# Performance work log

Measured on AMD Instinct MI355X. Metric: run time of the kernel, lower is better.

Reference implementation:

```python
import jax, jax.numpy as jnp
import numpy as np

B, S, D, H = 4, 2048, 1024, 16
HD = D // H  # head_dim = 64


def setup_inputs() -> dict:
    key = jax.random.key(0)
    ks = jax.random.split(key, 5)
    scale = 1.0 / np.sqrt(D)
    return {
        "x": jax.random.normal(ks[0], (B, S, D), dtype=jnp.float32),
        "Wq": jax.random.normal(ks[1], (D, D), dtype=jnp.float32) * scale,
        "bq": jnp.zeros((D,), dtype=jnp.float32),
        "Wk": jax.random.normal(ks[2], (D, D), dtype=jnp.float32) * scale,
        "bk": jnp.zeros((D,), dtype=jnp.float32),
        "Wv": jax.random.normal(ks[3], (D, D), dtype=jnp.float32) * scale,
        "bv": jnp.zeros((D,), dtype=jnp.float32),
        "Wp": jax.random.normal(ks[4], (D, D), dtype=jnp.float32) * scale,
        "bp": jnp.zeros((D,), dtype=jnp.float32),
    }


def reference(x, Wq, bq, Wk, bk, Wv, bv, Wp, bp):
    b, s, d = x.shape
    # qkv projections (torch Linear: x @ W.T + b; here W stored as (in,out))
    q = (x @ Wq + bq).reshape(b, s, H, HD).transpose(0, 2, 1, 3)  # (b,h,s,hd)
    k = (x @ Wk + bk).reshape(b, s, H, HD).transpose(0, 2, 1, 3)
    v = (x @ Wv + bv).reshape(b, s, H, HD).transpose(0, 2, 1, 3)
    scores = jnp.einsum("bhqd,bhkd->bhqk", q, k) / np.sqrt(HD)
    causal = jnp.tril(jnp.ones((s, s), dtype=bool))
    scores = jnp.where(causal, scores, -jnp.inf)
    attn = jax.nn.softmax(scores, axis=-1)  # dropout is identity (p=0 / eval)
    out = jnp.einsum("bhqk,bhkd->bhqd", attn, v)
    out = out.transpose(0, 2, 1, 3).reshape(b, s, d)
    return out @ Wp + bp
```

## Files before the change

### kernel.cpp

```cpp
#include <hip/hip_runtime.h>

typedef __bf16 bf16;
typedef __attribute__((ext_vector_type(4))) __bf16 bf16x4;
typedef __attribute__((ext_vector_type(8))) __bf16 bf16x8;
typedef __attribute__((ext_vector_type(4))) float f32x4;
typedef __attribute__((ext_vector_type(4))) unsigned int u32x4;

#define B_ 4
#define S_ 2048
#define D_ 1024
#define H_ 16
#define HD_ 64

#define GLB(p) ((const __attribute__((address_space(1))) void*)(p))
#define LDS(p) ((__attribute__((address_space(3))) void*)(p))

__global__ __launch_bounds__(256) void transpose_cvt(
    const float* __restrict__ W0, const float* __restrict__ W1,
    const float* __restrict__ W2, const float* __restrict__ W3,
    bf16* __restrict__ T0, bf16* __restrict__ T1,
    bf16* __restrict__ T2, bf16* __restrict__ T3)
{
    __shared__ float tile[32][33];
    int z = blockIdx.z;
    const float* W = (z == 0) ? W0 : (z == 1) ? W1 : (z == 2) ? W2 : W3;
    bf16*        T = (z == 0) ? T0 : (z == 1) ? T1 : (z == 2) ? T2 : T3;
    int bx = blockIdx.x * 32, by = blockIdx.y * 32;
    int tx = threadIdx.x & 31, ty = threadIdx.x >> 5;
    #pragma unroll
    for (int j = 0; j < 32; j += 8)
        tile[ty + j][tx] = W[(size_t)(by + ty + j) * D_ + bx + tx];
    __syncthreads();
    #pragma unroll
    for (int j = 0; j < 32; j += 8)
        T[(size_t)(bx + ty + j) * D_ + by + tx] = (bf16)tile[tx][ty + j];
}

__global__ __launch_bounds__(256) void cvt_x(
    const float* __restrict__ X, bf16* __restrict__ Xb)
{
    size_t i = ((size_t)blockIdx.x * 256 + threadIdx.x) * 8;
    f32x4 a = *(const f32x4*)(X + i);
    f32x4 b = *(const f32x4*)(X + i + 4);
    bf16x8 v;
    #pragma unroll
    for (int j = 0; j < 4; ++j) { v[j] = (bf16)a[j]; v[4 + j] = (bf16)b[j]; }
    *(bf16x8*)(Xb + i) = v;
}

__global__ __launch_bounds__(256) void qkv_gemm(
    const bf16* __restrict__ Xb,
    const bf16* __restrict__ WqT, const bf16* __restrict__ WkT, const bf16* __restrict__ WvT,
    const float* __restrict__ bq, const float* __restrict__ bk, const float* __restrict__ bv,
    bf16* __restrict__ Qo, bf16* __restrict__ Ko, bf16* __restrict__ Vo)
{
    const int z = blockIdx.z;
    const bf16*  WT   = (z == 0) ? WqT : (z == 1) ? WkT : WvT;
    const float* bias = (z == 0) ? bq  : (z == 1) ? bk  : bv;
    bf16*        out  = (z == 0) ? Qo  : (z == 1) ? Ko  : Vo;
    const float scale = (z == 0) ? 0.18033688011112042f : 1.0f;

    __shared__ bf16 As[128 * 32];
    __shared__ bf16 Bs[128 * 32];

    const int t = threadIdx.x;
    const int lid = t & 63, w = t >> 6;
    const int wm = w & 1, wn = w >> 1;
    const int lrow = lid & 15, quad = lid >> 4;
    const int m0 = blockIdx.y * 128, n0 = blockIdx.x * 128;

    const bf16* Ag = Xb + (size_t)m0 * D_;
    const bf16* Bg = WT + (size_t)n0 * D_;

    const int row0 = t >> 2, k80 = (t & 3) << 3;
    const int row1 = (t + 256) >> 2;

    f32x4 acc[4][4] = {};

    for (int k0 = 0; k0 < D_; k0 += 32) {
        __syncthreads();
        __builtin_amdgcn_global_load_lds(GLB(Ag + (size_t)row0 * D_ + k0 + k80),
                                         LDS(As + t * 8), 16, 0, 0);
        __builtin_amdgcn_global_load_lds(GLB(Bg + (size_t)row0 * D_ + k0 + k80),
                                         LDS(Bs + t * 8), 16, 0, 0);
        __builtin_amdgcn_global_load_lds(GLB(Ag + (size_t)row1 * D_ + k0 + k80),
                                         LDS(As + t * 8 + 2048), 16, 0, 0);
        __builtin_amdgcn_global_load_lds(GLB(Bg + (size_t)row1 * D_ + k0 + k80),
                                         LDS(Bs + t * 8 + 2048), 16, 0, 0);
        __syncthreads();
        bf16x8 a[4], b[4];
        #pragma unroll
        for (int mb = 0; mb < 4; ++mb)
            a[mb] = *(const bf16x8*)(As + (wm * 64 + mb * 16 + lrow) * 32 + quad * 8);
        #pragma unroll
        for (int nb = 0; nb < 4; ++nb)
            b[nb] = *(const bf16x8*)(Bs + (wn * 64 + nb * 16 + lrow) * 32 + quad * 8);
        #pragma unroll
        for (int mb = 0; mb < 4; ++mb)
            #pragma unroll
            for (int nb = 0; nb < 4; ++nb)
                acc[mb][nb] = __builtin_amdgcn_mfma_f32_16x16x32_bf16(a[mb], b[nb], acc[mb][nb], 0, 0, 0);
    }

    #pragma unroll
    for (int mb = 0; mb < 4; ++mb) {
        #pragma unroll
        for (int nb = 0; nb < 4; ++nb) {
            int gn = n0 + wn * 64 + nb * 16 + lrow;
            float bsv = bias[gn];
            int h = gn >> 6, hd = gn & 63;
            int gm0 = m0 + wm * 64 + mb * 16 + quad * 4;
            int bb = gm0 >> 11, s0 = gm0 & 2047;
            if (z == 2) {
                bf16x4 pk;
                #pragma unroll
                for (int r = 0; r < 4; ++r)
                    pk[r] = (bf16)(acc[mb][nb][r] + bsv);
                *(bf16x4*)(out + (((size_t)(bb * H_ + h)) * HD_ + hd) * S_ + s0) = pk;
            } else {
                #pragma unroll
                for (int r = 0; r < 4; ++r) {
                    float v = (acc[mb][nb][r] + bsv) * scale;
                    out[(((size_t)(bb * H_ + h)) * S_ + (s0 + r)) * HD_ + hd] = (bf16)v;
                }
            }
        }
    }
}

__global__ __launch_bounds__(256) void attn_fwd(
    const bf16* __restrict__ Q, const bf16* __restrict__ K,
    const bf16* __restrict__ Vt, bf16* __restrict__ O)
{
    __shared__ bf16 Ks[64 * 64];
    __shared__ bf16 Vs[64 * 64];
    __shared__ bf16 Ps[4][16 * 64];

    const int lin = blockIdx.x + (blockIdx.y << 4);
    const int xcd = lin & 7;
    const int sl  = lin >> 3;
    const int bh  = xcd * 8 + (sl >> 4);
    const int bxp = sl & 15;

    const int t = threadIdx.x, lid = t & 63, w = t >> 6;
    const int lrow = lid & 15, quad = lid >> 4;
    const int b = bh >> 4, h = bh & 15;

    const int swz = (lrow & 7) << 4;

    const int srow0 = t >> 3, srow1 = srow0 + 32;
    const int k8 = (t & 7) << 3;
    const int sswz = ((t & 7) << 4) ^ ((srow0 & 7) << 4);
    char* kdst0 = (char*)Ks + srow0 * 128 + sswz;
    char* kdst1 = (char*)Ks + srow1 * 128 + sswz;
    char* vdst0 = (char*)Vs + srow0 * 128 + sswz;
    char* vdst1 = (char*)Vs + srow1 * 128 + sswz;

    bf16x8 onesv;
    #pragma unroll
    for (int j = 0; j < 8; ++j) onesv[j] = (bf16)1.0f;

    #pragma unroll 1
    for (int half = 0; half < 2; ++half) {
        const int qtile = half ? bxp : (31 - bxp);
        const int qbase = qtile * 64;

        const bf16* Qp = Q + ((size_t)bh * S_ + qbase + w * 16) * HD_;
        bf16x8 qf[2];
        #pragma unroll
        for (int ks = 0; ks < 2; ++ks)
            qf[ks] = *(const bf16x8*)(Qp + lrow * HD_ + ks * 32 + quad * 8);

        f32x4 o_acc[4] = {};
        f32x4 l_acc = {0.0f, 0.0f, 0.0f, 0.0f};
        float m_i = -3.0e4f;

        for (int kt = 0; kt <= qtile; ++kt) {
            const bf16* Kp = K  + ((size_t)bh * S_ + kt * 64) * HD_;
            const bf16* Vp = Vt + ((size_t)bh * HD_) * S_ + kt * 64;
            __syncthreads();
            u32x4 kv0 = *(const u32x4*)(Kp + (size_t)srow0 * HD_ + k8);
            u32x4 kv1 = *(const u32x4*)(Kp + (size_t)srow1 * HD_ + k8);
            u32x4 vv0 = *(const u32x4*)(Vp + (size_t)srow0 * S_ + k8);
            u32x4 vv1 = *(const u32x4*)(Vp + (size_t)srow1 * S_ + k8);
            *(u32x4*)kdst0 = kv0;
            *(u32x4*)kdst1 = kv1;
            *(u32x4*)vdst0 = vv0;
            *(u32x4*)vdst1 = vv1;
            __syncthreads();

            f32x4 sa[4] = {};
            #pragma unroll
            for (int ks = 0; ks < 2; ++ks) {
                const int ro = ((ks << 6) + (quad << 4)) ^ swz;
                #pragma unroll
                for (int nb = 0; nb < 4; ++nb) {
                    bf16x8 kf = *(const bf16x8*)((const char*)Ks + (nb * 16 + lrow) * 128 + ro);
                    sa[nb] = __builtin_amdgcn_mfma_f32_16x16x32_bf16(kf, qf[ks], sa[nb], 0, 0, 0);
                }
            }

            if (kt == qtile) {
                int q = qbase + w * 16 + lrow;
                #pragma unroll
                for (int nb = 0; nb < 4; ++nb) {
                    int key = kt * 64 + nb * 16 + quad * 4;
                    #pragma unroll
                    for (int r = 0; r < 4; ++r)
                        if (key + r > q) sa[nb][r] = -3.0e4f;
                }
            }

            float p[4][4];
            {
                float r0 = fmaxf(fmaxf(sa[0][0], sa[0][1]), sa[0][2]);
                float r1 = fmaxf(fmaxf(sa[0][3], sa[1][0]), sa[1][1]);
                float r2 = fmaxf(fmaxf(sa[1][2], sa[1][3]), sa[2][0]);
                float r3 = fmaxf(fmaxf(sa[2][1], sa[2][2]), sa[2][3]);
                float r4 = fmaxf(fmaxf(sa[3][0], sa[3][1]), sa[3][2]);
                float rm = fmaxf(fmaxf(fmaxf(r0, r1), r2),
                                 fmaxf(fmaxf(r3, r4), sa[3][3]));
                rm = fmaxf(rm, __shfl_xor(rm, 16));
                rm = fmaxf(rm, __shfl_xor(rm, 32));
                const bool heavy = !__all(rm <= m_i + 8.0f);
                if (heavy) {
                    float mnew = fmaxf(m_i, rm);
                    float al = __builtin_amdgcn_exp2f(m_i - mnew);
                    m_i = mnew;
                    #pragma unroll
                    for (int nb = 0; nb < 4; ++nb)
                        #pragma unroll
                        for (int r = 0; r < 4; ++r)
                            o_acc[nb][r] *= al;
                    #pragma unroll
                    for (int r = 0; r < 4; ++r)
                        l_acc[r] *= al;
                }
                #pragma unroll
                for (int nb = 0; nb < 4; ++nb)
                    #pragma unroll
                    for (int r = 0; r < 4; ++r)
                        p[nb][r] = __builtin_amdgcn_exp2f(sa[nb][r] - m_i);
            }

            char* pw = (char*)Ps[w] + lrow * 128;
            #pragma unroll
            for (int nb = 0; nb < 4; ++nb) {
                bf16x4 pk;
                #pragma unroll
                for (int r = 0; r < 4; ++r)
                    pk[r] = (bf16)p[nb][r];
                *(bf16x4*)(pw + ((nb * 32 + quad * 8) ^ swz)) = pk;
            }
            asm volatile("s_waitcnt lgkmcnt(0)" ::: "memory");

            #pragma unroll
            for (int ks = 0; ks < 2; ++ks) {
                const int ro = ((ks << 6) + (quad << 4)) ^ swz;
                bf16x8 pf = *(const bf16x8*)(pw + ro);
                #pragma unroll
                for (int nb = 0; nb < 4; ++nb) {
                    bf16x8 vf = *(const bf16x8*)((const char*)Vs + (nb * 16 + lrow) * 128 + ro);
                    o_acc[nb] = __builtin_amdgcn_mfma_f32_16x16x32_bf16(vf, pf, o_acc[nb], 0, 0, 0);
                }
                l_acc = __builtin_amdgcn_mfma_f32_16x16x32_bf16(onesv, pf, l_acc, 0, 0, 0);
            }
        }

        {
            float inv = 1.0f / l_acc[0];
            int s = qbase + w * 16 + lrow;
            #pragma unroll
            for (int nb = 0; nb < 4; ++nb) {
                bf16x4 pk;
                #pragma unroll
                for (int r = 0; r < 4; ++r)
                    pk[r] = (bf16)(o_acc[nb][r] * inv);
                *(bf16x4*)(O + ((size_t)b * S_ + s) * D_ + h * 64 + nb * 16 + quad * 4) = pk;
            }
        }
        __syncthreads();
    }
}

__global__ __launch_bounds__(256) void proj_gemm(
    const bf16* __restrict__ A, const bf16* __restrict__ WpT,
    const float* __restrict__ bp, float* __restrict__ out)
{
    __shared__ bf16 As[128 * 32];
    __shared__ bf16 Bs[128 * 32];

    const int t = threadIdx.x;
    const int lid = t & 63, w = t >> 6;
    const int wm = w & 1, wn = w >> 1;
    const int lrow = lid & 15, quad = lid >> 4;
    const int m0 = blockIdx.y * 128, n0 = blockIdx.x * 128;

    const bf16* Ag = A   + (size_t)m0 * D_;
    const bf16* Bg = WpT + (size_t)n0 * D_;

    const int row0 = t >> 2, k80 = (t & 3) << 3;
    const int row1 = (t + 256) >> 2;

    f32x4 acc[4][4] = {};

    for (int k0 = 0; k0 < D_; k0 += 32) {
        __syncthreads();
        __builtin_amdgcn_global_load_lds(GLB(Ag + (size_t)row0 * D_ + k0 + k80),
                                         LDS(As + t * 8), 16, 0, 0);
        __builtin_amdgcn_global_load_lds(GLB(Bg + (size_t)row0 * D_ + k0 + k80),
                                         LDS(Bs + t * 8), 16, 0, 0);
        __builtin_amdgcn_global_load_lds(GLB(Ag + (size_t)row1 * D_ + k0 + k80),
                                         LDS(As + t * 8 + 2048), 16, 0, 0);
        __builtin_amdgcn_global_load_lds(GLB(Bg + (size_t)row1 * D_ + k0 + k80),
                                         LDS(Bs + t * 8 + 2048), 16, 0, 0);
        __syncthreads();
        bf16x8 a[4], b[4];
        #pragma unroll
        for (int mb = 0; mb < 4; ++mb)
            a[mb] = *(const bf16x8*)(As + (wm * 64 + mb * 16 + lrow) * 32 + quad * 8);
        #pragma unroll
        for (int nb = 0; nb < 4; ++nb)
            b[nb] = *(const bf16x8*)(Bs + (wn * 64 + nb * 16 + lrow) * 32 + quad * 8);
        #pragma unroll
        for (int mb = 0; mb < 4; ++mb)
            #pragma unroll
            for (int nb = 0; nb < 4; ++nb)
                acc[mb][nb] = __builtin_amdgcn_mfma_f32_16x16x32_bf16(a[mb], b[nb], acc[mb][nb], 0, 0, 0);
    }

    #pragma unroll
    for (int mb = 0; mb < 4; ++mb) {
        #pragma unroll
        for (int nb = 0; nb < 4; ++nb) {
            int gn = n0 + wn * 64 + nb * 16 + lrow;
            float bsv = bp[gn];
            #pragma unroll
            for (int r = 0; r < 4; ++r) {
                int gm = m0 + wm * 64 + mb * 16 + quad * 4 + r;
                out[(size_t)gm * D_ + gn] = acc[mb][nb][r] + bsv;
            }
        }
    }
}

extern "C" void kernel_launch(void* const* d_in, const int* in_sizes, int n_in,
                              void* d_out, int out_size, void* d_ws, size_t ws_size,
                              hipStream_t stream)
{
    const float* x  = (const float*)d_in[0];
    const float* Wq = (const float*)d_in[1];
    const float* bq = (const float*)d_in[2];
    const float* Wk = (const float*)d_in[3];
    const float* bk = (const float*)d_in[4];
    const float* Wv = (const float*)d_in[5];
    const float* bv = (const float*)d_in[6];
    const float* Wp = (const float*)d_in[7];
    const float* bp = (const float*)d_in[8];

    bf16* ws = (bf16*)d_ws;
    const size_t WSZ = (size_t)D_ * D_;
    const size_t BIG = (size_t)B_ * S_ * D_;
    bf16* WqT = ws;
    bf16* WkT = WqT + WSZ;
    bf16* WvT = WkT + WSZ;
    bf16* WpT = WvT + WSZ;
    bf16* Qb  = WpT + WSZ;
    bf16* Kb  = Qb + BIG;
    bf16* Vb  = Kb + BIG;
    bf16* Ab  = Vb + BIG;

    transpose_cvt<<<dim3(32, 32, 4), 256, 0, stream>>>(
        Wq, Wk, Wv, Wp, WqT, WkT, WvT, WpT);

    cvt_x<<<dim3(4096), 256, 0, stream>>>(x, Ab);

    qkv_gemm<<<dim3(8, 64, 3), 256, 0, stream>>>(
        Ab, WqT, WkT, WvT, bq, bk, bv, Qb, Kb, Vb);

    attn_fwd<<<dim3(16, 64), 256, 0, stream>>>(Qb, Kb, Vb, Ab);

    proj_gemm<<<dim3(8, 64), 256, 0, stream>>>(Ab, WpT, bp, (float*)d_out);
}
```

Baseline: 269.8 us.

## Widen GEMM K-tile to 64 with XOR-swizzled LDS and XCD-aware block remap

Both the QKV and projection GEMMs now stage a K-slice of 64 per iteration instead of 32. This halves the number of barrier pairs per tile and doubles the MFMA work between syncs. The LDS layout is XOR-swizzled on 16-byte chunks so that the 128-byte-stride row reads avoid bank conflicts. Block indices are also remapped so that consecutive blocks dispatched to the same XCD share M rows, improving L2 reuse. In exchange, LDS use per block doubles, and the remap hardcodes the grid shape (8 x 64 x 3).

```diff
diff --git a/kernel.cpp b/kernel.cpp
--- a/kernel.cpp
+++ b/kernel.cpp
@@ -54,52 +54,64 @@
     const float* __restrict__ bq, const float* __restrict__ bk, const float* __restrict__ bv,
     bf16* __restrict__ Qo, bf16* __restrict__ Ko, bf16* __restrict__ Vo)
 {
-    const int z = blockIdx.z;
+    const int lin = blockIdx.x + (blockIdx.y << 3) + (blockIdx.z << 9);
+    const int xcd = lin & 7, rest = lin >> 3;
+    const int byb = xcd * 8 + (rest & 7);
+    const int bxb = (rest >> 3) & 7;
+    const int z   = rest >> 6;
+
     const bf16*  WT   = (z == 0) ? WqT : (z == 1) ? WkT : WvT;
     const float* bias = (z == 0) ? bq  : (z == 1) ? bk  : bv;
     bf16*        out  = (z == 0) ? Qo  : (z == 1) ? Ko  : Vo;
     const float scale = (z == 0) ? 0.18033688011112042f : 1.0f;
 
-    __shared__ bf16 As[128 * 32];
-    __shared__ bf16 Bs[128 * 32];
+    __shared__ bf16 As[128 * 64];
+    __shared__ bf16 Bs[128 * 64];
 
     const int t = threadIdx.x;
     const int lid = t & 63, w = t >> 6;
     const int wm = w & 1, wn = w >> 1;
     const int lrow = lid & 15, quad = lid >> 4;
-    const int m0 = blockIdx.y * 128, n0 = blockIdx.x * 128;
+    const int m0 = byb * 128, n0 = bxb * 128;
 
     const bf16* Ag = Xb + (size_t)m0 * D_;
     const bf16* Bg = WT + (size_t)n0 * D_;
 
-    const int row0 = t >> 2, k80 = (t & 3) << 3;
-    const int row1 = (t + 256) >> 2;
+    const int srow = t >> 3;
+    const int ssel = ((t & 7) ^ (srow & 7)) << 3;
+
+    const int rsw = lrow & 7;
 
     f32x4 acc[4][4] = {};
 
-    for (int k0 = 0; k0 < D_; k0 += 32) {
+    for (int k0 = 0; k0 < D_; k0 += 64) {
         __syncthreads();
-        __builtin_amdgcn_global_load_lds(GLB(Ag + (size_t)row0 * D_ + k0 + k80),
-                                         LDS(As + t * 8), 16, 0, 0);
-        __builtin_amdgcn_global_load_lds(GLB(Bg + (size_t)row0 * D_ + k0 + k80),
-                                         LDS(Bs + t * 8), 16, 0, 0);
-        __builtin_amdgcn_global_load_lds(GLB(Ag + (size_t)row1 * D_ + k0 + k80),
-                                         LDS(As + t * 8 + 2048), 16, 0, 0);
-        __builtin_amdgcn_global_load_lds(GLB(Bg + (size_t)row1 * D_ + k0 + k80),
-                                         LDS(Bs + t * 8 + 2048), 16, 0, 0);
+        #pragma unroll
+        for (int j = 0; j < 4; ++j) {
+            __builtin_amdgcn_global_load_lds(
+                GLB(Ag + (size_t)(srow + j * 32) * D_ + k0 + ssel),
+                LDS((char*)As + j * 4096 + t * 16), 16, 0, 0);
+            __builtin_amdgcn_global_load_lds(
+                GLB(Bg + (size_t)(srow + j * 32) * D_ + k0 + ssel),
+                LDS((char*)Bs + j * 4096 + t * 16), 16, 0, 0);
+        }
         __syncthreads();
-        bf16x8 a[4], b[4];
-        #pragma unroll
-        for (int mb = 0; mb < 4; ++mb)
-            a[mb] = *(const bf16x8*)(As + (wm * 64 + mb * 16 + lrow) * 32 + quad * 8);
-        #pragma unroll
-        for (int nb = 0; nb < 4; ++nb)
-            b[nb] = *(const bf16x8*)(Bs + (wn * 64 + nb * 16 + lrow) * 32 + quad * 8);
-        #pragma unroll
-        for (int mb = 0; mb < 4; ++mb)
+        #pragma unroll
+        for (int kk = 0; kk < 2; ++kk) {
+            const int ro = ((kk * 4 + quad) ^ rsw) << 4;
+            bf16x8 a[4], b[4];
+            #pragma unroll
+            for (int mb = 0; mb < 4; ++mb)
+                a[mb] = *(const bf16x8*)((const char*)As + (wm * 64 + mb * 16 + lrow) * 128 + ro);
             #pragma unroll
             for (int nb = 0; nb < 4; ++nb)
-                acc[mb][nb] = __builtin_amdgcn_mfma_f32_16x16x32_bf16(a[mb], b[nb], acc[mb][nb], 0, 0, 0);
+                b[nb] = *(const bf16x8*)((const char*)Bs + (wn * 64 + nb * 16 + lrow) * 128 + ro);
+            #pragma unroll
+            for (int mb = 0; mb < 4; ++mb)
+                #pragma unroll
+                for (int nb = 0; nb < 4; ++nb)
+                    acc[mb][nb] = __builtin_amdgcn_mfma_f32_16x16x32_bf16(a[mb], b[nb], acc[mb][nb], 0, 0, 0);
+        }
     }
 
     #pragma unroll
@@ -287,46 +299,57 @@
     const bf16* __restrict__ A, const bf16* __restrict__ WpT,
     const float* __restrict__ bp, float* __restrict__ out)
 {
-    __shared__ bf16 As[128 * 32];
-    __shared__ bf16 Bs[128 * 32];
+    const int lin = blockIdx.x + (blockIdx.y << 3);
+    const int xcd = lin & 7, rest = lin >> 3;
+    const int byb = xcd * 8 + (rest & 7);
+    const int bxb = rest >> 3;
+
+    __shared__ bf16 As[128 * 64];
+    __shared__ bf16 Bs[128 * 64];
 
     const int t = threadIdx.x;
     const int lid = t & 63, w = t >> 6;
     const int wm = w & 1, wn = w >> 1;
     const int lrow = lid & 15, quad = lid >> 4;
-    const int m0 = blockIdx.y * 128, n0 = blockIdx.x * 128;
+    const int m0 = byb * 128, n0 = bxb * 128;
 
     const bf16* Ag = A   + (size_t)m0 * D_;
     const bf16* Bg = WpT + (size_t)n0 * D_;
 
-    const int row0 = t >> 2, k80 = (t & 3) << 3;
-    const int row1 = (t + 256) >> 2;
+    const int srow = t >> 3;
+    const int ssel = ((t & 7) ^ (srow & 7)) << 3;
+    const int rsw = lrow & 7;
 
     f32x4 acc[4][4] = {};
 
-    for (int k0 = 0; k0 < D_; k0 += 32) {
+    for (int k0 = 0; k0 < D_; k0 += 64) {
         __syncthreads();
-        __builtin_amdgcn_global_load_lds(GLB(Ag + (size_t)row0 * D_ + k0 + k80),
-                                         LDS(As + t * 8), 16, 0, 0);
-        __builtin_amdgcn_global_load_lds(GLB(Bg + (size_t)row0 * D_ + k0 + k80),
-                                         LDS(Bs + t * 8), 16, 0, 0);
-        __builtin_amdgcn_global_load_lds(GLB(Ag + (size_t)row1 * D_ + k0 + k80),
-                                         LDS(As + t * 8 + 2048), 16, 0, 0);
-        __builtin_amdgcn_global_load_lds(GLB(Bg + (size_t)row1 * D_ + k0 + k80),
-                                         LDS(Bs + t * 8 + 2048), 16, 0, 0);
+        #pragma unroll
+        for (int j = 0; j < 4; ++j) {
+            __builtin_amdgcn_global_load_lds(
+                GLB(Ag + (size_t)(srow + j * 32) * D_ + k0 + ssel),
+                LDS((char*)As + j * 4096 + t * 16), 16, 0, 0);
+            __builtin_amdgcn_global_load_lds(
+                GLB(Bg + (size_t)(srow + j * 32) * D_ + k0 + ssel),
+                LDS((char*)Bs + j * 4096 + t * 16), 16, 0, 0);
+        }
         __syncthreads();
-        bf16x8 a[4], b[4];
-        #pragma unroll
-        for (int mb = 0; mb < 4; ++mb)
-            a[mb] = *(const bf16x8*)(As + (wm * 64 + mb * 16 + lrow) * 32 + quad * 8);
-        #pragma unroll
-        for (int nb = 0; nb < 4; ++nb)
-            b[nb] = *(const bf16x8*)(Bs + (wn * 64 + nb * 16 + lrow) * 32 + quad * 8);
-        #pragma unroll
-        for (int mb = 0; mb < 4; ++mb)
+        #pragma unroll
+        for (int kk = 0; kk < 2; ++kk) {
+            const int ro = ((kk * 4 + quad) ^ rsw) << 4;
+            bf16x8 a[4], b[4];
+            #pragma unroll
+            for (int mb = 0; mb < 4; ++mb)
+                a[mb] = *(const bf16x8*)((const char*)As + (wm * 64 + mb * 16 + lrow) * 128 + ro);
             #pragma unroll
             for (int nb = 0; nb < 4; ++nb)
-                acc[mb][nb] = __builtin_amdgcn_mfma_f32_16x16x32_bf16(a[mb], b[nb], acc[mb][nb], 0, 0, 0);
+                b[nb] = *(const bf16x8*)((const char*)Bs + (wn * 64 + nb * 16 + lrow) * 128 + ro);
+            #pragma unroll
+            for (int mb = 0; mb < 4; ++mb)
+                #pragma unroll
+                for (int nb = 0; nb < 4; ++nb)
+                    acc[mb][nb] = __builtin_amdgcn_mfma_f32_16x16x32_bf16(a[mb], b[nb], acc[mb][nb], 0, 0, 0);
+        }
     }
 
     #pragma unroll
```

New measurement: 267.3 us. Within noise of the previous version (-0.9%).
